# Optimization experiments

Hardware: AMD Instinct MI355X
Metric: run time of the kernel (lower is better)

## Reference

```python
import jax, jax.numpy as jnp
import numpy as np

IN = 1    # input feature dim (hardcoded in NN)
H = 10    # LSTM hidden size (hardcoded in NN)
B = 8192  # batch
T = 256   # sequence length


def setup_inputs() -> dict:
    key = jax.random.key(0)
    ks = jax.random.split(key, 12)
    s = 0.1  # init scale for mus (mimics blitz posterior_mu_init spread)
    RHO0 = -3.0  # posterior_rho_init from the module
    return {
        "x": jax.random.normal(ks[0], (B, T, IN), jnp.float32),
        # BayesianLSTM variational parameters (blitz layout: (in, 4*H), (H, 4*H), (4*H,))
        "w_ih_mu": jax.random.normal(ks[1], (IN, 4 * H), jnp.float32) * s,
        "w_ih_rho": jnp.full((IN, 4 * H), RHO0, jnp.float32),
        "w_hh_mu": jax.random.normal(ks[2], (H, 4 * H), jnp.float32) * s,
        "w_hh_rho": jnp.full((H, 4 * H), RHO0, jnp.float32),
        "b_mu": jax.random.normal(ks[3], (4 * H,), jnp.float32) * s,
        "b_rho": jnp.full((4 * H,), RHO0, jnp.float32),
        # reparameterization noise, sampled once per forward call in blitz
        "eps_ih": jax.random.normal(ks[4], (IN, 4 * H), jnp.float32),
        "eps_hh": jax.random.normal(ks[5], (H, 4 * H), jnp.float32),
        "eps_b": jax.random.normal(ks[6], (4 * H,), jnp.float32),
        # deterministic linear head nn.Linear(10, 1)
        "lin_w": jax.random.normal(ks[7], (1, H), jnp.float32) * s,
        "lin_b": jnp.zeros((1,), jnp.float32),
    }


def reference(x, w_ih_mu, w_ih_rho, w_hh_mu, w_hh_rho, b_mu, b_rho,
              eps_ih, eps_hh, eps_b, lin_w, lin_b):
    sp = jax.nn.softplus
    # sample weights: w = mu + log1p(exp(rho)) * eps
    w_ih = w_ih_mu + sp(w_ih_rho) * eps_ih   # (IN, 4H)
    w_hh = w_hh_mu + sp(w_hh_rho) * eps_hh   # (H, 4H)
    b = b_mu + sp(b_rho) * eps_b             # (4H,)

    # precompute input contribution for all timesteps: (B, T, 4H)
    x_proj = jnp.einsum('bti,ig->btg', x, w_ih) + b

    def step(carry, xg):
        h, c = carry                      # (B, H) each
        gates = xg + h @ w_hh             # (B, 4H)
        i = jax.nn.sigmoid(gates[:, :H])
        f = jax.nn.sigmoid(gates[:, H:2 * H])
        g = jnp.tanh(gates[:, 2 * H:3 * H])
        o = jax.nn.sigmoid(gates[:, 3 * H:])
        c = f * c + i * g
        h = o * jnp.tanh(c)
        return (h, c), None

    h0 = jnp.zeros((x.shape[0], H), x.dtype)
    (h_last, _), _ = jax.lax.scan(step, (h0, h0), jnp.swapaxes(x_proj, 0, 1))
    # NN takes hidden_seq[:, -1, :] == final hidden state, then linear head
    return h_last @ lin_w.T + lin_b  # (B, 1)
```

## Files before the change

kernel.cpp:

```cpp
#include <hip/hip_runtime.h>
#include <math.h>

#define T_LEN 256
#define HID 10

typedef float v2f __attribute__((ext_vector_type(2)));

template <int PAT>
__device__ __forceinline__ float swz(float v) {
    return __int_as_float(__builtin_amdgcn_ds_swizzle(__float_as_int(v), PAT));
}

__device__ __forceinline__ float softplus_f(float x) {
    return fmaxf(x, 0.0f) + log1pf(expf(-fabsf(x)));
}
__device__ __forceinline__ float samp(const float* mu, const float* rho,
                                      const float* eps, int i) {
    return mu[i] + softplus_f(rho[i]) * eps[i];
}

__device__ __forceinline__ float fast_sigmoid(float x) {
    float e = __builtin_amdgcn_exp2f(-1.442695040888963f * x);
    return __builtin_amdgcn_rcpf(1.0f + e);
}
__device__ __forceinline__ float fast_tanh(float x) {
    float e = __builtin_amdgcn_exp2f(2.885390081777927f * x);
    return fmaf(-2.0f, __builtin_amdgcn_rcpf(e + 1.0f), 1.0f);
}

#define DOTJ(J, HV)                                                    \
    hh.x = hh.y = (HV);                                                \
    a01 = __builtin_elementwise_fma(hh, whh01[J], a01);                \
    a23 = __builtin_elementwise_fma(hh, whh23[J], a23);

#define ELEM_STEP(H0, H1, H2, XV, CC, HK, HB, WR)                      \
    {                                                                  \
        v2f hh;                                                        \
        hh.x = hh.y = (XV);                                            \
        v2f a01 = __builtin_elementwise_fma(hh, wih01, bb01);          \
        v2f a23 = __builtin_elementwise_fma(hh, wih23, bb23);          \
        DOTJ(0, (H0).x) DOTJ(1, (H0).y) DOTJ(2, (H0).z) DOTJ(3, (H0).w)\
        DOTJ(4, (H1).x) DOTJ(5, (H1).y) DOTJ(6, (H1).z) DOTJ(7, (H1).w)\
        DOTJ(8, (H2).x) DOTJ(9, (H2).y)                                \
        float si = fast_sigmoid(a01.x);                                \
        float sf = fast_sigmoid(a01.y);                                \
        float tg = fast_tanh(a23.x);                                   \
        float so = fast_sigmoid(a23.y);                                \
        (CC) = fmaf(sf, (CC), si * tg);                                \
        (HK) = so * fast_tanh(CC);                                     \
        (WR)[0] = (HK);                                                \
        (H0) = *(const float4*)(HB);                                   \
        (H1) = *(const float4*)((HB) + 4);                             \
        (H2) = *(const float2*)((HB) + 8);                             \
    }

__global__ __launch_bounds__(256) void bayes_lstm_kernel(
    const float* __restrict__ x,
    const float* __restrict__ w_ih_mu, const float* __restrict__ w_ih_rho,
    const float* __restrict__ w_hh_mu, const float* __restrict__ w_hh_rho,
    const float* __restrict__ b_mu,    const float* __restrict__ b_rho,
    const float* __restrict__ eps_ih,  const float* __restrict__ eps_hh,
    const float* __restrict__ eps_b,
    const float* __restrict__ lin_w,   const float* __restrict__ lin_b,
    float* __restrict__ out)
{
    __shared__ __align__(16) float hbuf[16 * 2 * 20];

    const int tid  = threadIdx.x;
    const int k    = tid & 15;
    const int slot = tid >> 4;
    const int bA   = (blockIdx.x * 16 + slot) * 2;
    const int bB   = bA + 1;

    float* hbA = hbuf + (slot * 2 + 0) * 20;
    float* hbB = hbuf + (slot * 2 + 1) * 20;
    float* wrA = hbA + k;
    float* wrB = hbB + k;

    v2f whh01[HID], whh23[HID];
    v2f wih01, wih23, bb01, bb23;
    wih01.x = wih01.y = 0.f; wih23.x = wih23.y = 0.f;
    bb01.x = bb01.y = 0.f;   bb23.x = bb23.y = 0.f;
    float lw = 0.f;
#pragma unroll
    for (int j = 0; j < HID; ++j) {
        whh01[j].x = whh01[j].y = 0.f;
        whh23[j].x = whh23[j].y = 0.f;
    }
    if (k < HID) {
        const int c0 = k, c1 = HID + k, c2 = 2 * HID + k, c3 = 3 * HID + k;
        wih01.x = samp(w_ih_mu, w_ih_rho, eps_ih, c0);
        wih01.y = samp(w_ih_mu, w_ih_rho, eps_ih, c1);
        wih23.x = samp(w_ih_mu, w_ih_rho, eps_ih, c2);
        wih23.y = samp(w_ih_mu, w_ih_rho, eps_ih, c3);
        bb01.x  = samp(b_mu, b_rho, eps_b, c0);
        bb01.y  = samp(b_mu, b_rho, eps_b, c1);
        bb23.x  = samp(b_mu, b_rho, eps_b, c2);
        bb23.y  = samp(b_mu, b_rho, eps_b, c3);
#pragma unroll
        for (int j = 0; j < HID; ++j) {
            whh01[j].x = samp(w_hh_mu, w_hh_rho, eps_hh, j * 4 * HID + c0);
            whh01[j].y = samp(w_hh_mu, w_hh_rho, eps_hh, j * 4 * HID + c1);
            whh23[j].x = samp(w_hh_mu, w_hh_rho, eps_hh, j * 4 * HID + c2);
            whh23[j].y = samp(w_hh_mu, w_hh_rho, eps_hh, j * 4 * HID + c3);
        }
        lw = lin_w[k];
    }

    float4 hA0 = {0,0,0,0}, hA1 = {0,0,0,0};
    float4 hB0 = {0,0,0,0}, hB1 = {0,0,0,0};
    float2 hA2v = {0,0}, hB2v = {0,0};
    float cA = 0.f, cB = 0.f, hkA = 0.f, hkB = 0.f;

    const float* xrA = x + (size_t)bA * T_LEN;
    const float* xrB = x + (size_t)bB * T_LEN;
    float xA0 = xrA[0], xA1 = xrA[1];
    float xB0 = xrB[0], xB1 = xrB[1];

#pragma unroll 16
    for (int t = 0; t < T_LEN; ++t) {
        float xA2 = xrA[(t + 2) & (T_LEN - 1)];
        float xB2 = xrB[(t + 2) & (T_LEN - 1)];
        ELEM_STEP(hA0, hA1, hA2v, xA0, cA, hkA, hbA, wrA)
        ELEM_STEP(hB0, hB1, hB2v, xB0, cB, hkB, hbB, wrB)
        xA0 = xA1; xA1 = xA2;
        xB0 = xB1; xB1 = xB2;
    }

    float pa = hkA * lw;
    float pb = hkB * lw;
    pa += swz<(1 << 10) | 0x1f>(pa);  pb += swz<(1 << 10) | 0x1f>(pb);
    pa += swz<(2 << 10) | 0x1f>(pa);  pb += swz<(2 << 10) | 0x1f>(pb);
    pa += swz<(4 << 10) | 0x1f>(pa);  pb += swz<(4 << 10) | 0x1f>(pb);
    pa += swz<(8 << 10) | 0x1f>(pa);  pb += swz<(8 << 10) | 0x1f>(pb);
    if (k == 0) {
        float b0 = lin_b[0];
        out[bA] = pa + b0;
        out[bB] = pb + b0;
    }
}

extern "C" void kernel_launch(void* const* d_in, const int* in_sizes, int n_in,
                              void* d_out, int out_size, void* d_ws, size_t ws_size,
                              hipStream_t stream) {
    const float* x        = (const float*)d_in[0];
    const float* w_ih_mu  = (const float*)d_in[1];
    const float* w_ih_rho = (const float*)d_in[2];
    const float* w_hh_mu  = (const float*)d_in[3];
    const float* w_hh_rho = (const float*)d_in[4];
    const float* b_mu     = (const float*)d_in[5];
    const float* b_rho    = (const float*)d_in[6];
    const float* eps_ih   = (const float*)d_in[7];
    const float* eps_hh   = (const float*)d_in[8];
    const float* eps_b    = (const float*)d_in[9];
    const float* lin_w    = (const float*)d_in[10];
    const float* lin_b    = (const float*)d_in[11];
    float* out = (float*)d_out;

    const int n_b = in_sizes[0] / T_LEN;
    dim3 grid(n_b / 32), block(256);
    hipLaunchKernelGGL(bayes_lstm_kernel, grid, block, 0, stream,
                       x, w_ih_mu, w_ih_rho, w_hh_mu, w_hh_rho, b_mu, b_rho,
                       eps_ih, eps_hh, eps_b, lin_w, lin_b, out);
}
```

Before: 177.4 us.

## Broadcast hidden state via ds_swizzle instead of LDS round-trip; coalesce x loads

The per-step LDS write and read-back of the hidden vector is replaced by ten ds_swizzle broadcasts within each 16-lane group, removing the shared-memory buffer. Input x is now loaded coalesced, 16 timesteps at a time with one element per lane, then broadcast per step with swizzle. This removes LDS store/load latency from the serial recurrence and the scalar per-step x loads. In exchange it issues more swizzle instructions per step, and ds_swizzle still goes through the LDS crossbar path.

```diff
diff --git a/kernel.cpp b/kernel.cpp
--- a/kernel.cpp
+++ b/kernel.cpp
@@ -33,25 +33,39 @@
     a01 = __builtin_elementwise_fma(hh, whh01[J], a01);                \
     a23 = __builtin_elementwise_fma(hh, whh23[J], a23);
 
-#define ELEM_STEP(H0, H1, H2, XV, CC, HK, HB, WR)                      \
+#define ELEM_STEP(HA, XV, CC, HK)                                      \
     {                                                                  \
         v2f hh;                                                        \
         hh.x = hh.y = (XV);                                            \
         v2f a01 = __builtin_elementwise_fma(hh, wih01, bb01);          \
         v2f a23 = __builtin_elementwise_fma(hh, wih23, bb23);          \
-        DOTJ(0, (H0).x) DOTJ(1, (H0).y) DOTJ(2, (H0).z) DOTJ(3, (H0).w)\
-        DOTJ(4, (H1).x) DOTJ(5, (H1).y) DOTJ(6, (H1).z) DOTJ(7, (H1).w)\
-        DOTJ(8, (H2).x) DOTJ(9, (H2).y)                                \
+        DOTJ(0, HA[0]) DOTJ(1, HA[1]) DOTJ(2, HA[2]) DOTJ(3, HA[3])    \
+        DOTJ(4, HA[4]) DOTJ(5, HA[5]) DOTJ(6, HA[6]) DOTJ(7, HA[7])    \
+        DOTJ(8, HA[8]) DOTJ(9, HA[9])                                  \
         float si = fast_sigmoid(a01.x);                                \
         float sf = fast_sigmoid(a01.y);                                \
         float tg = fast_tanh(a23.x);                                   \
         float so = fast_sigmoid(a23.y);                                \
         (CC) = fmaf(sf, (CC), si * tg);                                \
         (HK) = so * fast_tanh(CC);                                     \
-        (WR)[0] = (HK);                                                \
-        (H0) = *(const float4*)(HB);                                   \
-        (H1) = *(const float4*)((HB) + 4);                             \
-        (H2) = *(const float2*)((HB) + 8);                             \
+        HA[0] = swz<(0 << 5) | 0x10>(HK);                              \
+        HA[1] = swz<(1 << 5) | 0x10>(HK);                              \
+        HA[2] = swz<(2 << 5) | 0x10>(HK);                              \
+        HA[3] = swz<(3 << 5) | 0x10>(HK);                              \
+        HA[4] = swz<(4 << 5) | 0x10>(HK);                              \
+        HA[5] = swz<(5 << 5) | 0x10>(HK);                              \
+        HA[6] = swz<(6 << 5) | 0x10>(HK);                              \
+        HA[7] = swz<(7 << 5) | 0x10>(HK);                              \
+        HA[8] = swz<(8 << 5) | 0x10>(HK);                              \
+        HA[9] = swz<(9 << 5) | 0x10>(HK);                              \
+    }
+
+#define TSTEP(TI)                                                      \
+    {                                                                  \
+        float xa = swz<((TI) << 5) | 0x10>(xcA);                       \
+        float xb = swz<((TI) << 5) | 0x10>(xcB);                       \
+        ELEM_STEP(hA, xa, cA, hkA)                                     \
+        ELEM_STEP(hB, xb, cB, hkB)                                     \
     }
 
 __global__ __launch_bounds__(256) void bayes_lstm_kernel(
@@ -64,18 +78,11 @@
     const float* __restrict__ lin_w,   const float* __restrict__ lin_b,
     float* __restrict__ out)
 {
-    __shared__ __align__(16) float hbuf[16 * 2 * 20];
-
     const int tid  = threadIdx.x;
     const int k    = tid & 15;
     const int slot = tid >> 4;
     const int bA   = (blockIdx.x * 16 + slot) * 2;
     const int bB   = bA + 1;
-
-    float* hbA = hbuf + (slot * 2 + 0) * 20;
-    float* hbB = hbuf + (slot * 2 + 1) * 20;
-    float* wrA = hbA + k;
-    float* wrB = hbB + k;
 
     v2f whh01[HID], whh23[HID];
     v2f wih01, wih23, bb01, bb23;
@@ -107,24 +114,27 @@
         lw = lin_w[k];
     }
 
-    float4 hA0 = {0,0,0,0}, hA1 = {0,0,0,0};
-    float4 hB0 = {0,0,0,0}, hB1 = {0,0,0,0};
-    float2 hA2v = {0,0}, hB2v = {0,0};
+    float hA[HID], hB[HID];
+#pragma unroll
+    for (int j = 0; j < HID; ++j) { hA[j] = 0.f; hB[j] = 0.f; }
     float cA = 0.f, cB = 0.f, hkA = 0.f, hkB = 0.f;
 
     const float* xrA = x + (size_t)bA * T_LEN;
     const float* xrB = x + (size_t)bB * T_LEN;
-    float xA0 = xrA[0], xA1 = xrA[1];
-    float xB0 = xrB[0], xB1 = xrB[1];
+    float xcA = xrA[k];
+    float xcB = xrB[k];
 
-#pragma unroll 16
-    for (int t = 0; t < T_LEN; ++t) {
-        float xA2 = xrA[(t + 2) & (T_LEN - 1)];
-        float xB2 = xrB[(t + 2) & (T_LEN - 1)];
-        ELEM_STEP(hA0, hA1, hA2v, xA0, cA, hkA, hbA, wrA)
-        ELEM_STEP(hB0, hB1, hB2v, xB0, cB, hkB, hbB, wrB)
-        xA0 = xA1; xA1 = xA2;
-        xB0 = xB1; xB1 = xB2;
+    for (int to = 0; to < 16; ++to) {
+        float xnA = 0.f, xnB = 0.f;
+        if (to < 15) {
+            xnA = xrA[(to + 1) * 16 + k];
+            xnB = xrB[(to + 1) * 16 + k];
+        }
+        TSTEP(0)  TSTEP(1)  TSTEP(2)  TSTEP(3)
+        TSTEP(4)  TSTEP(5)  TSTEP(6)  TSTEP(7)
+        TSTEP(8)  TSTEP(9)  TSTEP(10) TSTEP(11)
+        TSTEP(12) TSTEP(13) TSTEP(14) TSTEP(15)
+        xcA = xnA; xcB = xnB;
     }
 
     float pa = hkA * lw;
```

Result: slower. 185.6 us (+4.6%).
